# Kernel tuning notes

Measured on AMD Instinct MI355X. Metric: run time of the kernel, lower is better.

## Reference

```python
import jax, jax.numpy as jnp
import numpy as np

B, T, VT, E, D = 128, 512, 2048, 1024, 1024  # batch, num_topics, topic_vocab, enc_hid, dec_hid


def setup_inputs() -> dict:
    key = jax.random.key(0)
    ks = jax.random.split(key, 8)
    # Split the Linear weight (in = dec_hid + topic_vocab + enc_hid, concat order: hidden, topic, enc)
    # into per-input blocks; math is identical to Linear(cat([h, t, e])).
    s = 1.0 / np.sqrt(D + VT + E)
    return {
        "hidden": jax.random.normal(ks[0], (B, D), jnp.float32),
        "topic_dict": jax.random.uniform(ks[1], (T, VT), jnp.float32),
        "enc_hidden": jax.random.normal(ks[2], (B, E), jnp.float32),
        "W_h": jax.random.uniform(ks[3], (D, D), jnp.float32, -s, s),
        "W_t": jax.random.uniform(ks[4], (VT, D), jnp.float32, -s, s),
        "W_e": jax.random.uniform(ks[5], (E, D), jnp.float32, -s, s),
        "b": jax.random.uniform(ks[6], (D,), jnp.float32, -s, s),
        "v": jax.random.uniform(ks[7], (D,), jnp.float32),
    }


def reference(hidden, topic_dict, enc_hidden, W_h, W_t, W_e, b, v):
    # Decompose Linear(cat(h, t, e)) = h@W_h + t@W_t + e@W_e + b; avoids the
    # repeated/concatenated [B, T, D+VT+E] buffer while computing the same math.
    h_proj = hidden @ W_h          # [B, D]
    t_proj = topic_dict @ W_t      # [T, D]
    e_proj = enc_hidden @ W_e      # [B, D]
    energy = jnp.tanh(h_proj[:, None, :] + e_proj[:, None, :] + t_proj[None, :, :] + b)  # [B, T, D]
    score = jnp.einsum("btd,d->bt", energy, v)  # [B, T]
    return jax.nn.softmax(score, axis=1)[:, None, :]  # [B, 1, T]
```

## Files before the change

kernel.cpp:

```cpp
#include <hip/hip_runtime.h>
#include <hip/hip_fp16.h>

#define B_ 128
#define T_ 512
#define VT_ 2048
#define E_ 1024
#define D_ 1024

typedef _Float16 h8 __attribute__((ext_vector_type(8)));
typedef float f4 __attribute__((ext_vector_type(4)));

#define C2LE 2.8853900817779268f
#define L2E  1.4426950408889634f

static __device__ __forceinline__ float rcpf(float x) { return __builtin_amdgcn_rcpf(x); }
static __device__ __forceinline__ float ex2(float x)  { return __builtin_amdgcn_exp2f(x); }

#define R_FLOATS   (640 * 1024)
#define SP_FLOATS  (8 * 128 * 512)
#define PA_HALVES  (640 * 2048)
#define PB_WH      0
#define PB_WE      1048576
#define PB_WT      2097152

__device__ __forceinline__ void pack_panelA(const float* __restrict__ src, int ld,
                                            _Float16* __restrict__ dst, int mb_off, int kb_off,
                                            int pm, int pk, int tid, float lds[64][72])
{
    #pragma unroll
    for (int p = 0; p < 4; ++p) {
        int row = (tid >> 4) + p * 16, col = (tid & 15) * 4;
        *(f4*)&lds[row][col] = *(const f4*)&src[(size_t)(pm * 64 + row) * ld + pk * 64 + col];
    }
    __syncthreads();
    #pragma unroll
    for (int w = 0; w < 2; ++w) {
        int fl = w * 256 + tid;
        int f = fl >> 6, lane = fl & 63;
        int i = f >> 1, k2 = f & 1;
        int r = lane & 15, g = lane >> 4;
        const float* p = &lds[i * 16 + r][k2 * 32 + g * 8];
        h8 h;
        #pragma unroll
        for (int j = 0; j < 8; ++j) h[j] = (_Float16)p[j];
        int MB = mb_off + pm * 4 + i;
        int KB = kb_off + pk * 2 + k2;
        *(h8*)(dst + ((size_t)(MB * 64 + KB) * 64 + lane) * 8) = h;
    }
}

__device__ __forceinline__ void pack_panelB(const float* __restrict__ W,
                                            _Float16* __restrict__ dst, int KBdim,
                                            int pk, int pn, int tid, float lds[64][72])
{
    #pragma unroll
    for (int p = 0; p < 4; ++p) {
        int row = (tid >> 4) + p * 16, col = (tid & 15) * 4;
        *(f4*)&lds[row][col] = *(const f4*)&W[(size_t)(pk * 64 + row) * 1024 + pn * 64 + col];
    }
    __syncthreads();
    #pragma unroll
    for (int w = 0; w < 2; ++w) {
        int fl = w * 256 + tid;
        int f = fl >> 6, lane = fl & 63;
        int j = f >> 1, i2 = f & 1;
        int r = lane & 15, g = lane >> 4;
        h8 h;
        #pragma unroll
        for (int jj = 0; jj < 8; ++jj) h[jj] = (_Float16)lds[i2 * 32 + g * 8 + jj][j * 16 + r];
        int NB = pn * 4 + j;
        int KB = pk * 2 + i2;
        *(h8*)(dst + ((size_t)(NB * KBdim + KB) * 64 + lane) * 8) = h;
    }
}

__global__ __launch_bounds__(256) void pack_kernel(
    const float* __restrict__ hidden, const float* __restrict__ topic,
    const float* __restrict__ enc,
    const float* __restrict__ W_h, const float* __restrict__ W_t, const float* __restrict__ W_e,
    _Float16* __restrict__ pA, _Float16* __restrict__ pB)
{
    __shared__ float lds[64][72];
    const int bid = blockIdx.x, tid = threadIdx.x;
    if (bid < 32) {
        int b = bid;        pack_panelA(hidden, 1024, pA, 0,  0, b >> 4, b & 15, tid, lds);
    } else if (bid < 64) {
        int b = bid - 32;   pack_panelA(enc,    1024, pA, 0, 32, b >> 4, b & 15, tid, lds);
    } else if (bid < 320) {
        int b = bid - 64;   pack_panelA(topic,  2048, pA, 8,  0, b >> 5, b & 31, tid, lds);
    } else if (bid < 576) {
        int b = bid - 320;  pack_panelB(W_h, pB + PB_WH, 32, b >> 4, b & 15, tid, lds);
    } else if (bid < 832) {
        int b = bid - 576;  pack_panelB(W_e, pB + PB_WE, 32, b >> 4, b & 15, tid, lds);
    } else {
        int b = bid - 832;  pack_panelB(W_t, pB + PB_WT, 64, b >> 4, b & 15, tid, lds);
    }
}

__global__ __launch_bounds__(256, 3) void gemm_kernel(const _Float16* __restrict__ pA,
                                                      const _Float16* __restrict__ pB,
                                                      float* __restrict__ R)
{
    const int lin = blockIdx.x;
    const int sw  = (lin & 7) * 80 + (lin >> 3);
    const int s   = sw / 80;
    const int rem = sw % 80;
    const int mt  = rem % 10;
    const int nt  = rem / 10;

    const int tid = threadIdx.x, wave = tid >> 6, lane = tid & 63;
    const int wm = (wave >> 1) * 32;
    const int wn = (wave & 1) * 64;
    const int r = lane & 15, g = lane >> 4;

    const int mb0 = mt * 4 + (wm >> 4);
    const int nb0 = (nt * 128 + wn) >> 4;
    const int kb0 = s * 8;

    const _Float16* Bp; int KB_B, kbB0;
    if (mt < 2) {
        if (kb0 < 32) { Bp = pB + PB_WH; kbB0 = kb0; }
        else          { Bp = pB + PB_WE; kbB0 = kb0 - 32; }
        KB_B = 32;
    } else { Bp = pB + PB_WT; kbB0 = kb0; KB_B = 64; }

    const _Float16* Ap = pA + ((size_t)(mb0 * 64 + kb0) * 64 + lane) * 8;
    const _Float16* Bq = Bp + ((size_t)(nb0 * KB_B + kbB0) * 64 + lane) * 8;
    const size_t aStrM = (size_t)64 * 512;
    const size_t bStrN = (size_t)KB_B * 512;

    f4 acc[2][4] = {};
    #pragma unroll
    for (int ks = 0; ks < 8; ++ks) {
        h8 a0 = *(const h8*)(Ap + (size_t)ks * 512);
        h8 a1 = *(const h8*)(Ap + aStrM + (size_t)ks * 512);
        h8 b0 = *(const h8*)(Bq + (size_t)ks * 512);
        h8 b1 = *(const h8*)(Bq + bStrN + (size_t)ks * 512);
        h8 b2 = *(const h8*)(Bq + 2 * bStrN + (size_t)ks * 512);
        h8 b3 = *(const h8*)(Bq + 3 * bStrN + (size_t)ks * 512);
        acc[0][0] = __builtin_amdgcn_mfma_f32_16x16x32_f16(a0, b0, acc[0][0], 0, 0, 0);
        acc[0][1] = __builtin_amdgcn_mfma_f32_16x16x32_f16(a0, b1, acc[0][1], 0, 0, 0);
        acc[0][2] = __builtin_amdgcn_mfma_f32_16x16x32_f16(a0, b2, acc[0][2], 0, 0, 0);
        acc[0][3] = __builtin_amdgcn_mfma_f32_16x16x32_f16(a0, b3, acc[0][3], 0, 0, 0);
        acc[1][0] = __builtin_amdgcn_mfma_f32_16x16x32_f16(a1, b0, acc[1][0], 0, 0, 0);
        acc[1][1] = __builtin_amdgcn_mfma_f32_16x16x32_f16(a1, b1, acc[1][1], 0, 0, 0);
        acc[1][2] = __builtin_amdgcn_mfma_f32_16x16x32_f16(a1, b2, acc[1][2], 0, 0, 0);
        acc[1][3] = __builtin_amdgcn_mfma_f32_16x16x32_f16(a1, b3, acc[1][3], 0, 0, 0);
    }

    float* Rp = R + ((size_t)(mt * 64 + wm + g * 4)) * 1024 + nt * 128 + wn + r;
    #pragma unroll
    for (int i = 0; i < 2; ++i)
        #pragma unroll
        for (int j = 0; j < 4; ++j)
            #pragma unroll
            for (int q = 0; q < 4; ++q)
                atomicAdd(&Rp[(size_t)(i * 16 + q) * 1024 + j * 16], C2LE * acc[i][j][q]);
}

__global__ __launch_bounds__(256) void score_kernel(const float* __restrict__ R,
                                                    const float* __restrict__ bias,
                                                    const float* __restrict__ v,
                                                    float* __restrict__ SP)
{
    __shared__ float Xs[16][128];
    __shared__ float Ys[64][128];
    __shared__ float vs[128];

    const int tid = threadIdx.x;
    const int b0 = blockIdx.x * 16;
    const int t0 = blockIdx.y * 64;
    const int d0 = blockIdx.z * 128;

    #pragma unroll
    for (int i = 0; i < 8; ++i) {
        int idx = tid + i * 256;
        int row = idx >> 5, c4 = idx & 31;
        f4 vv = *(const f4*)&R[(size_t)(128 + t0 + row) * 1024 + d0 + c4 * 4];
        *(f4*)&Ys[row][(c4 ^ (row & 15)) * 4] = vv;
    }
    #pragma unroll
    for (int i = 0; i < 2; ++i) {
        int idx = tid + i * 256;
        int row = idx >> 5, c4 = idx & 31;
        f4 vv = *(const f4*)&R[(size_t)(b0 + row) * 1024 + d0 + c4 * 4];
        f4 bb = *(const f4*)&bias[d0 + c4 * 4];
        vv += bb * C2LE;
        *(f4*)&Xs[row][(c4 ^ (row & 15)) * 4] = vv;
    }
    if (tid < 32) *(f4*)&vs[tid * 4] = *(const f4*)&v[d0 + tid * 4];
    __syncthreads();

    const int tq = tid & 31, bq = tid >> 5;
    const int sx0 = bq & 15, sx1 = (bq + 8) & 15, sy = tq & 15;
    float a00 = 0.f, a01 = 0.f, a10 = 0.f, a11 = 0.f;

    for (int dd = 0; dd < 32; ++dd) {
        f4 xa = *(const f4*)&Xs[bq]     [(dd ^ sx0) * 4];
        f4 xb = *(const f4*)&Xs[bq + 8] [(dd ^ sx1) * 4];
        f4 ya = *(const f4*)&Ys[tq]     [(dd ^ sy) * 4];
        f4 yb = *(const f4*)&Ys[tq + 32][(dd ^ sy) * 4];
        f4 vv = *(const f4*)&vs[dd * 4];
        #pragma unroll
        for (int j = 0; j < 4; ++j) {
            float e;
            e = ex2(xa[j] + ya[j]); a00 += vv[j] * rcpf(e + 1.0f);
            e = ex2(xa[j] + yb[j]); a01 += vv[j] * rcpf(e + 1.0f);
            e = ex2(xb[j] + ya[j]); a10 += vv[j] * rcpf(e + 1.0f);
            e = ex2(xb[j] + yb[j]); a11 += vv[j] * rcpf(e + 1.0f);
        }
    }

    float* sp = SP + (size_t)blockIdx.z * (B_ * T_);
    sp[(size_t)(b0 + bq)     * T_ + t0 + tq]      = a00;
    sp[(size_t)(b0 + bq)     * T_ + t0 + tq + 32] = a01;
    sp[(size_t)(b0 + bq + 8) * T_ + t0 + tq]      = a10;
    sp[(size_t)(b0 + bq + 8) * T_ + t0 + tq + 32] = a11;
}

__global__ __launch_bounds__(256) void softmax_kernel(
    const float* __restrict__ SP, float* __restrict__ out)
{
    const int b = blockIdx.x, tid = threadIdx.x;
    float s0 = 0.f, s1 = 0.f;
    #pragma unroll
    for (int z = 0; z < 8; ++z) {
        s0 += SP[(size_t)z * B_ * T_ + (size_t)b * T_ + tid];
        s1 += SP[(size_t)z * B_ * T_ + (size_t)b * T_ + tid + 256];
    }
    s0 *= -2.0f; s1 *= -2.0f;

    float m = fmaxf(s0, s1);
    #pragma unroll
    for (int off = 32; off >= 1; off >>= 1) m = fmaxf(m, __shfl_xor(m, off));
    __shared__ float red[4];
    __shared__ float red2[4];
    const int wv = tid >> 6;
    if ((tid & 63) == 0) red[wv] = m;
    __syncthreads();
    m = fmaxf(fmaxf(red[0], red[1]), fmaxf(red[2], red[3]));

    float e0 = ex2((s0 - m) * L2E);
    float e1 = ex2((s1 - m) * L2E);
    float sum = e0 + e1;
    #pragma unroll
    for (int off = 32; off >= 1; off >>= 1) sum += __shfl_xor(sum, off);
    if ((tid & 63) == 0) red2[wv] = sum;
    __syncthreads();
    sum = red2[0] + red2[1] + red2[2] + red2[3];

    const float rs = rcpf(sum);
    out[(size_t)b * T_ + tid]       = e0 * rs;
    out[(size_t)b * T_ + tid + 256] = e1 * rs;
}

extern "C" void kernel_launch(void* const* d_in, const int* in_sizes, int n_in,
                              void* d_out, int out_size, void* d_ws, size_t ws_size,
                              hipStream_t stream)
{
    const float* hidden = (const float*)d_in[0];
    const float* topic  = (const float*)d_in[1];
    const float* enc    = (const float*)d_in[2];
    const float* W_h    = (const float*)d_in[3];
    const float* W_t    = (const float*)d_in[4];
    const float* W_e    = (const float*)d_in[5];
    const float* bvec   = (const float*)d_in[6];
    const float* vvec   = (const float*)d_in[7];
    float* out = (float*)d_out;

    float* R      = (float*)d_ws;
    float* SPb    = R + R_FLOATS;
    _Float16* pA  = (_Float16*)(SPb + SP_FLOATS);
    _Float16* pB  = pA + PA_HALVES;

    (void)hipMemsetAsync(R, 0, R_FLOATS * sizeof(float), stream);
    pack_kernel<<<1344, 256, 0, stream>>>(hidden, topic, enc, W_h, W_t, W_e, pA, pB);
    gemm_kernel<<<640, 256, 0, stream>>>(pA, pB, R);
    score_kernel<<<dim3(8, 8, 8), 256, 0, stream>>>(R, bvec, vvec, SPb);
    softmax_kernel<<<128, 256, 0, stream>>>(SPb, out);
}
```

Measured before the change: 124.5 us.

## Replace atomic split-K accumulation with partial buffers and a separate reduce kernel

The GEMM now writes each split-K slice's partial tile to its own slice of a workspace buffer instead of atomically adding into a shared result. A new reduce kernel sums the eight partials and folds in the scaled bias, so the memset and the bias add in the score kernel are dropped. This removes atomic contention and the memset launch. In exchange it adds an extra kernel launch and roughly 20 MB of partial-buffer traffic.

```diff
diff --git a/kernel.cpp b/kernel.cpp
--- a/kernel.cpp
+++ b/kernel.cpp
@@ -16,6 +16,7 @@
 static __device__ __forceinline__ float rcpf(float x) { return __builtin_amdgcn_rcpf(x); }
 static __device__ __forceinline__ float ex2(float x)  { return __builtin_amdgcn_exp2f(x); }
 
+#define P_FLOATS   (8 * 640 * 1024)
 #define R_FLOATS   (640 * 1024)
 #define SP_FLOATS  (8 * 128 * 512)
 #define PA_HALVES  (640 * 2048)
@@ -99,7 +100,7 @@
 
 __global__ __launch_bounds__(256, 3) void gemm_kernel(const _Float16* __restrict__ pA,
                                                       const _Float16* __restrict__ pB,
-                                                      float* __restrict__ R)
+                                                      float* __restrict__ P)
 {
     const int lin = blockIdx.x;
     const int sw  = (lin & 7) * 80 + (lin >> 3);
@@ -148,18 +149,34 @@
         acc[1][3] = __builtin_amdgcn_mfma_f32_16x16x32_f16(a1, b3, acc[1][3], 0, 0, 0);
     }
 
-    float* Rp = R + ((size_t)(mt * 64 + wm + g * 4)) * 1024 + nt * 128 + wn + r;
+    float* Pp = P + ((size_t)s * 640 + mt * 64 + wm + g * 4) * 1024 + nt * 128 + wn + r;
     #pragma unroll
     for (int i = 0; i < 2; ++i)
         #pragma unroll
         for (int j = 0; j < 4; ++j)
             #pragma unroll
             for (int q = 0; q < 4; ++q)
-                atomicAdd(&Rp[(size_t)(i * 16 + q) * 1024 + j * 16], C2LE * acc[i][j][q]);
+                Pp[(size_t)(i * 16 + q) * 1024 + j * 16] = C2LE * acc[i][j][q];
+}
+
+__global__ __launch_bounds__(256) void reduce_kernel(const float* __restrict__ P,
+                                                     const float* __restrict__ bias,
+                                                     float* __restrict__ R)
+{
+    const int row = blockIdx.x, tid = threadIdx.x;
+    const size_t off = (size_t)row * 1024 + tid * 4;
+    const size_t PS = (size_t)640 * 1024;
+    f4 acc = *(const f4*)&P[off];
+    #pragma unroll
+    for (int z = 1; z < 8; ++z) acc += *(const f4*)&P[off + (size_t)z * PS];
+    if (row < 128) {
+        f4 bb = *(const f4*)&bias[tid * 4];
+        acc += bb * C2LE;
+    }
+    *(f4*)&R[off] = acc;
 }
 
 __global__ __launch_bounds__(256) void score_kernel(const float* __restrict__ R,
-                                                    const float* __restrict__ bias,
                                                     const float* __restrict__ v,
                                                     float* __restrict__ SP)
 {
@@ -184,8 +201,6 @@
         int idx = tid + i * 256;
         int row = idx >> 5, c4 = idx & 31;
         f4 vv = *(const f4*)&R[(size_t)(b0 + row) * 1024 + d0 + c4 * 4];
-        f4 bb = *(const f4*)&bias[d0 + c4 * 4];
-        vv += bb * C2LE;
         *(f4*)&Xs[row][(c4 ^ (row & 15)) * 4] = vv;
     }
     if (tid < 32) *(f4*)&vs[tid * 4] = *(const f4*)&v[d0 + tid * 4];
@@ -268,14 +283,15 @@
     const float* vvec   = (const float*)d_in[7];
     float* out = (float*)d_out;
 
-    float* R      = (float*)d_ws;
+    float* P      = (float*)d_ws;
+    float* R      = P + P_FLOATS;
     float* SPb    = R + R_FLOATS;
     _Float16* pA  = (_Float16*)(SPb + SP_FLOATS);
     _Float16* pB  = pA + PA_HALVES;
 
-    (void)hipMemsetAsync(R, 0, R_FLOATS * sizeof(float), stream);
     pack_kernel<<<1344, 256, 0, stream>>>(hidden, topic, enc, W_h, W_t, W_e, pA, pB);
-    gemm_kernel<<<640, 256, 0, stream>>>(pA, pB, R);
-    score_kernel<<<dim3(8, 8, 8), 256, 0, stream>>>(R, bvec, vvec, SPb);
+    gemm_kernel<<<640, 256, 0, stream>>>(pA, pB, P);
+    reduce_kernel<<<640, 256, 0, stream>>>(P, bvec, R);
+    score_kernel<<<dim3(8, 8, 8), 256, 0, stream>>>(R, vvec, SPb);
     softmax_kernel<<<128, 256, 0, stream>>>(SPb, out);
 }
```

Result: faster. 115.8 us (-7.0%).
